# Optimization experiments

Measured on AMD Instinct MI355X. Metric: run time of the kernel, lower is better.

## Reference

```python
import jax, jax.numpy as jnp
import numpy as np

B, H, W, C = 16, 128, 128, 128
Wh = Ww = 8
SH = 4  # shift size
NH = 4  # heads
HD = C // NH
N = Wh * Ww
HID = 4 * C
EPS = 1e-3  # keras LayerNormalization default epsilon
SCALE = HD ** -0.5


def _rel_pos_index():
    coords = np.stack(np.meshgrid(np.arange(Wh), np.arange(Ww), indexing='ij'))  # (2,Wh,Ww)
    flat = coords.reshape(2, -1)
    rel = flat[:, :, None] - flat[:, None, :]  # (2,N,N)
    rel = rel.transpose(1, 2, 0) + np.array([Wh - 1, Ww - 1])
    rel = rel * np.array([2 * Ww - 1, 1])
    return rel.sum(-1).astype(np.int32)  # (N,N)


def _attn_mask():
    img = np.zeros((1, H, W, 1))
    h_sl = (slice(0, H - Wh), slice(H - Wh, H - SH), slice(H - SH, H))
    w_sl = (slice(0, W - Ww), slice(W - Ww, W - SH), slice(W - SH, W))
    cnt = 0
    for hs in h_sl:
        for ws in w_sl:
            img[:, hs, ws, :] = cnt
            cnt += 1
    mw = img.reshape(1, H // Wh, Wh, W // Ww, Ww, 1).transpose(0, 1, 3, 2, 4, 5).reshape(-1, N)
    am = mw[:, None, :] - mw[:, :, None]
    return np.where(am != 0, -100.0, 0.0).astype(np.float32)  # (nW,N,N)


def setup_inputs() -> dict:
    key = jax.random.key(0)
    ks = jax.random.split(key, 12)
    s = 0.02
    return {
        'x': jax.random.normal(ks[0], (B, H * W, C), jnp.float32),
        'w_qkv': jax.random.normal(ks[1], (C, 3 * C), jnp.float32) * s,
        'b_qkv': jnp.zeros((3 * C,), jnp.float32),
        'bias_table': jax.random.normal(ks[2], ((2 * Wh - 1) * (2 * Ww - 1), NH), jnp.float32) * s,
        'w_proj': jax.random.normal(ks[3], (C, C), jnp.float32) * s,
        'b_proj': jnp.zeros((C,), jnp.float32),
        'g1': jnp.ones((C,), jnp.float32),
        'be1': jnp.zeros((C,), jnp.float32),
        'w_fc1': jax.random.normal(ks[4], (C, HID), jnp.float32) * s,
        'b_fc1': jnp.zeros((HID,), jnp.float32),
        'w_fc2': jax.random.normal(ks[5], (HID, C), jnp.float32) * s,
        'b_fc2': jnp.zeros((C,), jnp.float32),
        'g2': jnp.ones((C,), jnp.float32),
        'be2': jnp.zeros((C,), jnp.float32),
        'rel_index': jnp.asarray(_rel_pos_index()),
        'attn_mask': jnp.asarray(_attn_mask()),
    }


def _ln(x, g, b):
    m = jnp.mean(x, -1, keepdims=True)
    v = jnp.mean(jnp.square(x - m), -1, keepdims=True)
    return (x - m) * jax.lax.rsqrt(v + EPS) * g + b


def _block(x, w_qkv, b_qkv, bias_table, w_proj, b_proj, g1, be1,
           w_fc1, b_fc1, w_fc2, b_fc2, g2, be2, rel_index, attn_mask):
    xi = x.reshape(B, H, W, C)
    xs = jnp.roll(xi, (-SH, -SH), axis=(1, 2))
    # window partition -> (B*nW, N, C)
    xw = xs.reshape(B, H // Wh, Wh, W // Ww, Ww, C).transpose(0, 1, 3, 2, 4, 5).reshape(-1, N, C)
    qkv = (xw @ w_qkv + b_qkv).reshape(-1, N, 3, NH, HD).transpose(2, 0, 3, 1, 4)
    q, k, v = qkv[0] * SCALE, qkv[1], qkv[2]
    attn = jnp.einsum('bhnd,bhmd->bhnm', q, k)  # (B*nW, NH, N, N)
    rpb = bias_table[rel_index.reshape(-1)].reshape(N, N, NH).transpose(2, 0, 1)
    attn = attn + rpb[None]
    nW = attn_mask.shape[0]
    attn = attn.reshape(-1, nW, NH, N, N) + attn_mask[None, :, None]
    attn = jax.nn.softmax(attn.reshape(-1, NH, N, N), axis=-1)
    out = jnp.einsum('bhnm,bhmd->bhnd', attn, v).transpose(0, 2, 1, 3).reshape(-1, N, C)
    out = out @ w_proj + b_proj
    # window reverse + unshift
    out = out.reshape(B, H // Wh, W // Ww, Wh, Ww, C).transpose(0, 1, 3, 2, 4, 5).reshape(B, H, W, C)
    out = jnp.roll(out, (SH, SH), axis=(1, 2)).reshape(B, H * W, C)
    # NOTE: this module applies norm AFTER the sublayers (post-norm residual)
    x = x + _ln(out, g1, be1)
    h = jax.nn.gelu(x @ w_fc1 + b_fc1, approximate=False) @ w_fc2 + b_fc2
    x = x + _ln(h, g2, be2)
    return x


def reference(x, w_qkv, b_qkv, bias_table, w_proj, b_proj, g1, be1,
              w_fc1, b_fc1, w_fc2, b_fc2, g2, be2, rel_index, attn_mask):
    return _block(x, w_qkv, b_qkv, bias_table, w_proj, b_proj, g1, be1,
                  w_fc1, b_fc1, w_fc2, b_fc2, g2, be2, rel_index, attn_mask)
```

## Files before the change

kernel.cpp:

```cpp
#include <hip/hip_runtime.h>
#include <hip/hip_bf16.h>
#include <math.h>

typedef unsigned short u16;
typedef unsigned int   u32;

typedef __bf16 bf16x8 __attribute__((ext_vector_type(8)));
typedef float  f32x4  __attribute__((ext_vector_type(4)));
#define MFMA_B16 __builtin_amdgcn_mfma_f32_16x16x32_bf16

__device__ __forceinline__ u16 f2b(float f) {
    union { float f; u32 i; } v; v.f = f;
    u32 x = v.i;
    u32 r = x + 0x7fffu + ((x >> 16) & 1u);
    return (u16)(r >> 16);
}
__device__ __forceinline__ u32 pk2(float a, float b) {
    return (u32)f2b(a) | ((u32)f2b(b) << 16);
}
__device__ __forceinline__ bf16x8 pk8(float4 f0, float4 f1) {
    union { u32 u[4]; bf16x8 v; } cv;
    cv.u[0] = pk2(f0.x, f0.y); cv.u[1] = pk2(f0.z, f0.w);
    cv.u[2] = pk2(f1.x, f1.y); cv.u[3] = pk2(f1.z, f1.w);
    return cv.v;
}

__device__ __forceinline__ float gelu_fast(float v) {
    const float z = v * (1.5957691f + 0.07135486f * v * v);
    return v * __builtin_amdgcn_rcpf(1.0f + __expf(-z));
}

#define SCALE_ 0.17677669529663687f
#define EPS_   1e-3f


__global__ __launch_bounds__(256) void swin_prep(
    const float* __restrict__ w_qkv, const float* __restrict__ w_proj,
    const float* __restrict__ w_fc1, const float* __restrict__ w_fc2,
    const float* __restrict__ bias_table, const int* __restrict__ rel_index,
    const float* __restrict__ attn_mask,
    u16* __restrict__ wqkvT, u16* __restrict__ wprojT,
    u16* __restrict__ w1T, u16* __restrict__ w2T, float* __restrict__ rpbm)
{
    const int idx = blockIdx.x * 256 + threadIdx.x;
    if (idx < 49152) {
        const int o = idx >> 7, c = idx & 127;
        wqkvT[idx] = f2b(w_qkv[c * 384 + o]);
    } else if (idx < 65536) {
        const int i2 = idx - 49152;
        const int o = i2 >> 7, c = i2 & 127;
        wprojT[i2] = f2b(w_proj[c * 128 + o]);
    } else if (idx < 131072) {
        const int i2 = idx - 65536;
        const int o = i2 >> 7, c = i2 & 127;
        w1T[i2] = f2b(w_fc1[c * 512 + o]);
    } else if (idx < 196608) {
        const int i2 = idx - 131072;
        const int o = i2 >> 9, u = i2 & 511;
        w2T[i2] = f2b(w_fc2[u * 128 + o]);
    } else if (idx < 262144) {
        const int i2 = idx - 196608;
        const int cls = i2 >> 14, rem = i2 & 16383;
        const int h = rem >> 12, ij = rem & 4095;
        const int widx = ((cls & 2) ? 240 : 0) + ((cls & 1) ? 15 : 0);
        rpbm[i2] = bias_table[rel_index[ij] * 4 + h] + attn_mask[widx * 4096 + ij];
    }
}

#define QA_OFF 0
#define KA_OFF 10240
#define VA_OFF 20480
#define PA_OFF 0
#define AO_OFF 0
#define X2F_OFF 4352

__global__ __launch_bounds__(256) void swin_attn_mfma(
    const float* __restrict__ x, const u16* __restrict__ wqkvT, const float* __restrict__ b_qkv,
    const u16* __restrict__ wprojT, const float* __restrict__ b_proj,
    const float* __restrict__ g1, const float* __restrict__ be1,
    const float* __restrict__ rpbm, float* __restrict__ x1out)
{
    __shared__ __align__(16) u16 sm[29696];
    const int tid  = threadIdx.x;
    const int w    = tid >> 6;
    const int lane = tid & 63;
    const int l15  = lane & 15;
    const int quad = lane >> 4;
    const int win  = blockIdx.x;
    const int b = win >> 8, wr = (win >> 4) & 15, wc = win & 15;

    size_t rowb[4];
    #pragma unroll
    for (int mi = 0; mi < 4; mi++) {
        const int t  = mi * 16 + l15;
        const int hh = (wr * 8 + (t >> 3) + 4) & 127;
        const int ww = (wc * 8 + (t & 7) + 4) & 127;
        rowb[mi] = ((size_t)((b * 128 + hh) * 128 + ww)) * 128;
    }

    {
        f32x4 acc[6][4];
        #pragma unroll
        for (int n = 0; n < 6; n++) {
            const float bq = b_qkv[w * 96 + n * 16 + l15];
            #pragma unroll
            for (int mi = 0; mi < 4; mi++) acc[n][mi] = (f32x4){bq, bq, bq, bq};
        }
        #pragma unroll
        for (int ks = 0; ks < 4; ks++) {
            bf16x8 a[4], bb[6];
            #pragma unroll
            for (int mi = 0; mi < 4; mi++) {
                const float4 f0 = *(const float4*)(x + rowb[mi] + ks * 32 + quad * 8);
                const float4 f1 = *(const float4*)(x + rowb[mi] + ks * 32 + quad * 8 + 4);
                a[mi] = pk8(f0, f1);
            }
            #pragma unroll
            for (int n = 0; n < 6; n++)
                bb[n] = *(const bf16x8*)(wqkvT + (size_t)(w * 96 + n * 16 + l15) * 128 + ks * 32 + quad * 8);
            #pragma unroll
            for (int n = 0; n < 6; n++)
                #pragma unroll
                for (int mi = 0; mi < 4; mi++)
                    acc[n][mi] = MFMA_B16(a[mi], bb[n], acc[n][mi], 0, 0, 0);
        }
        #pragma unroll
        for (int n = 0; n < 6; n++) {
            const int o = w * 96 + n * 16 + l15;
            const int s = o >> 7, h = (o >> 5) & 3, d = o & 31;
            #pragma unroll
            for (int mi = 0; mi < 4; mi++) {
                if (s < 2) {
                    const int base = (s ? KA_OFF : QA_OFF) + h * 2560 + d;
                    const float sc = s ? 1.0f : SCALE_;
                    #pragma unroll
                    for (int r = 0; r < 4; r++)
                        sm[base + (mi * 16 + quad * 4 + r) * 40] = f2b(acc[n][mi][r] * sc);
                } else {
                    const int t0 = mi * 16 + quad * 4;
                    const u32 w0 = pk2(acc[n][mi][0], acc[n][mi][1]);
                    const u32 w1 = pk2(acc[n][mi][2], acc[n][mi][3]);
                    *(uint2*)(sm + VA_OFF + h * 2304 + d * 72 + t0) = make_uint2(w0, w1);
                }
            }
        }
    }
    __syncthreads();

    float sinv[4][4];
    {
        const int h = w;
        const float* rb = rpbm + (size_t)((((wr == 15) ? 2 : 0) | ((wc == 15) ? 1 : 0)) * 4 + h) * 4096;
        f32x4 S[4][4];
        #pragma unroll
        for (int mi = 0; mi < 4; mi++)
            #pragma unroll
            for (int ni = 0; ni < 4; ni++)
                #pragma unroll
                for (int r = 0; r < 4; r++)
                    S[mi][ni][r] = rb[(mi * 16 + quad * 4 + r) * 64 + ni * 16 + l15];
        bf16x8 aq[4], bk[4];
        #pragma unroll
        for (int mi = 0; mi < 4; mi++)
            aq[mi] = *(const bf16x8*)(sm + QA_OFF + h * 2560 + (mi * 16 + l15) * 40 + quad * 8);
        #pragma unroll
        for (int ni = 0; ni < 4; ni++)
            bk[ni] = *(const bf16x8*)(sm + KA_OFF + h * 2560 + (ni * 16 + l15) * 40 + quad * 8);
        #pragma unroll
        for (int mi = 0; mi < 4; mi++)
            #pragma unroll
            for (int ni = 0; ni < 4; ni++)
                S[mi][ni] = MFMA_B16(aq[mi], bk[ni], S[mi][ni], 0, 0, 0);
        #pragma unroll
        for (int mi = 0; mi < 4; mi++) {
            #pragma unroll
            for (int r = 0; r < 4; r++) {
                float m0 = fmaxf(fmaxf(S[mi][0][r], S[mi][1][r]), fmaxf(S[mi][2][r], S[mi][3][r]));
                m0 = fmaxf(m0, __shfl_xor(m0, 1));
                m0 = fmaxf(m0, __shfl_xor(m0, 2));
                m0 = fmaxf(m0, __shfl_xor(m0, 4));
                m0 = fmaxf(m0, __shfl_xor(m0, 8));
                float s0 = 0.0f;
                #pragma unroll
                for (int ni = 0; ni < 4; ni++) {
                    const float e = __expf(S[mi][ni][r] - m0);
                    S[mi][ni][r] = e;
                    s0 += e;
                }
                s0 += __shfl_xor(s0, 1);
                s0 += __shfl_xor(s0, 2);
                s0 += __shfl_xor(s0, 4);
                s0 += __shfl_xor(s0, 8);
                sinv[mi][r] = __builtin_amdgcn_rcpf(s0);
            }
        }
        __syncthreads();

        #pragma unroll
        for (int mi = 0; mi < 4; mi++)
            #pragma unroll
            for (int ni = 0; ni < 4; ni++)
                #pragma unroll
                for (int r = 0; r < 4; r++)
                    sm[PA_OFF + h * 4608 + (mi * 16 + quad * 4 + r) * 72 + ni * 16 + l15] = f2b(S[mi][ni][r]);

        f32x4 O[4][2];
        #pragma unroll
        for (int mi = 0; mi < 4; mi++)
            #pragma unroll
            for (int ni = 0; ni < 2; ni++) O[mi][ni] = (f32x4){0.f, 0.f, 0.f, 0.f};
        #pragma unroll
        for (int ks = 0; ks < 2; ks++) {
            bf16x8 ap[4], bv[2];
            #pragma unroll
            for (int mi = 0; mi < 4; mi++)
                ap[mi] = *(const bf16x8*)(sm + PA_OFF + h * 4608 + (mi * 16 + l15) * 72 + ks * 32 + quad * 8);
            #pragma unroll
            for (int ni = 0; ni < 2; ni++)
                bv[ni] = *(const bf16x8*)(sm + VA_OFF + h * 2304 + (ni * 16 + l15) * 72 + ks * 32 + quad * 8);
            #pragma unroll
            for (int mi = 0; mi < 4; mi++)
                #pragma unroll
                for (int ni = 0; ni < 2; ni++)
                    O[mi][ni] = MFMA_B16(ap[mi], bv[ni], O[mi][ni], 0, 0, 0);
        }
        __syncthreads();

        #pragma unroll
        for (int mi = 0; mi < 4; mi++)
            #pragma unroll
            for (int ni = 0; ni < 2; ni++)
                #pragma unroll
                for (int r = 0; r < 4; r++)
                    sm[AO_OFF + (mi * 16 + quad * 4 + r) * 136 + h * 32 + ni * 16 + l15]
                        = f2b(O[mi][ni][r] * sinv[mi][r]);
    }
    __syncthreads();

    {
        f32x4 X2[4][2];
        #pragma unroll
        for (int ni = 0; ni < 2; ni++) {
            const float bp = b_proj[w * 32 + ni * 16 + l15];
            #pragma unroll
            for (int mi = 0; mi < 4; mi++) X2[mi][ni] = (f32x4){bp, bp, bp, bp};
        }
        #pragma unroll
        for (int ks = 0; ks < 4; ks++) {
            bf16x8 aa[4], bw[2];
            #pragma unroll
            for (int mi = 0; mi < 4; mi++)
                aa[mi] = *(const bf16x8*)(sm + AO_OFF + (mi * 16 + l15) * 136 + ks * 32 + quad * 8);
            #pragma unroll
            for (int ni = 0; ni < 2; ni++)
                bw[ni] = *(const bf16x8*)(wprojT + (size_t)(w * 32 + ni * 16 + l15) * 128 + ks * 32 + quad * 8);
            #pragma unroll
            for (int mi = 0; mi < 4; mi++)
                #pragma unroll
                for (int ni = 0; ni < 2; ni++)
                    X2[mi][ni] = MFMA_B16(aa[mi], bw[ni], X2[mi][ni], 0, 0, 0);
        }
        float* X2f = (float*)sm + X2F_OFF;
        #pragma unroll
        for (int mi = 0; mi < 4; mi++)
            #pragma unroll
            for (int ni = 0; ni < 2; ni++)
                #pragma unroll
                for (int r = 0; r < 4; r++)
                    X2f[(mi * 16 + quad * 4 + r) * 132 + w * 32 + ni * 16 + l15] = X2[mi][ni][r];
    }
    __syncthreads();

    {
        const int t = tid >> 2, part = tid & 3;
        const float* Xr = (const float*)sm + X2F_OFF + t * 132 + part * 32;
        float4 xr[8];
        float s1 = 0.f, s2 = 0.f;
        #pragma unroll
        for (int k = 0; k < 8; k++) {
            xr[k] = *(const float4*)(Xr + k * 4);
            s1 += xr[k].x + xr[k].y + xr[k].z + xr[k].w;
            s2 += xr[k].x * xr[k].x + xr[k].y * xr[k].y
                + xr[k].z * xr[k].z + xr[k].w * xr[k].w;
        }
        s1 += __shfl_xor(s1, 1); s1 += __shfl_xor(s1, 2);
        s2 += __shfl_xor(s2, 1); s2 += __shfl_xor(s2, 2);
        const float m  = s1 * 0.0078125f;
        const float vr = fmaxf(s2 * 0.0078125f - m * m, 0.f);
        const float rs = rsqrtf(vr + EPS_);
        const int hh = (wr * 8 + (t >> 3) + 4) & 127;
        const int ww = (wc * 8 + (t & 7) + 4) & 127;
        const size_t g = ((size_t)((b * 128 + hh) * 128 + ww)) * 128 + part * 32;
        #pragma unroll
        for (int k = 0; k < 8; k++) {
            const int c4 = k * 4;
            const float4 xv = *(const float4*)(x + g + c4);
            const float4 gv = *(const float4*)(g1 + part * 32 + c4);
            const float4 bv = *(const float4*)(be1 + part * 32 + c4);
            float4 o;
            o.x = xv.x + (xr[k].x - m) * rs * gv.x + bv.x;
            o.y = xv.y + (xr[k].y - m) * rs * gv.y + bv.y;
            o.z = xv.z + (xr[k].z - m) * rs * gv.z + bv.z;
            o.w = xv.w + (xr[k].w - m) * rs * gv.w + bv.w;
            *(float4*)(x1out + g + c4) = o;
        }
    }
}

#define HB_OFF 8704
#define X3F_OFF 4352

__global__ __launch_bounds__(256) void swin_mlp_mfma(
    float* __restrict__ x1io, const u16* __restrict__ w1T, const float* __restrict__ b_fc1,
    const u16* __restrict__ w2T, const float* __restrict__ b_fc2,
    const float* __restrict__ g2, const float* __restrict__ be2)
{
    __shared__ __align__(16) u16 sm[25600];
    const int tid  = threadIdx.x;
    const int w    = tid >> 6;
    const int lane = tid & 63;
    const int l15  = lane & 15;
    const int quad = lane >> 4;
    const size_t base = (size_t)blockIdx.x * 8192;

    for (int e = tid * 8; e < 8192; e += 2048) {
        const int t = e >> 7, c = e & 127;
        const float4 f0 = *(const float4*)(x1io + base + e);
        const float4 f1 = *(const float4*)(x1io + base + e + 4);
        union { bf16x8 v; uint4 u; } cv; cv.v = pk8(f0, f1);
        *(uint4*)(sm + t * 136 + c) = cv.u;
    }
    __syncthreads();

    f32x4 acc2[2][4];
    #pragma unroll
    for (int ni = 0; ni < 2; ni++) {
        const float bb = b_fc2[w * 32 + ni * 16 + l15];
        #pragma unroll
        for (int mi = 0; mi < 4; mi++) acc2[ni][mi] = (f32x4){bb, bb, bb, bb};
    }

    for (int ch = 0; ch < 2; ch++) {
        f32x4 a1[4][4];
        #pragma unroll
        for (int ni = 0; ni < 4; ni++) {
            const float bb = b_fc1[ch * 256 + (w * 4 + ni) * 16 + l15];
            #pragma unroll
            for (int mi = 0; mi < 4; mi++) a1[ni][mi] = (f32x4){bb, bb, bb, bb};
        }
        #pragma unroll
        for (int ks = 0; ks < 4; ks++) {
            bf16x8 af[4], bf[4];
            #pragma unroll
            for (int mi = 0; mi < 4; mi++)
                af[mi] = *(const bf16x8*)(sm + (mi * 16 + l15) * 136 + ks * 32 + quad * 8);
            #pragma unroll
            for (int ni = 0; ni < 4; ni++)
                bf[ni] = *(const bf16x8*)(w1T + (size_t)(ch * 256 + (w * 4 + ni) * 16 + l15) * 128 + ks * 32 + quad * 8);
            #pragma unroll
            for (int ni = 0; ni < 4; ni++)
                #pragma unroll
                for (int mi = 0; mi < 4; mi++)
                    a1[ni][mi] = MFMA_B16(af[mi], bf[ni], a1[ni][mi], 0, 0, 0);
        }
        #pragma unroll
        for (int ni = 0; ni < 4; ni++)
            #pragma unroll
            for (int mi = 0; mi < 4; mi++)
                #pragma unroll
                for (int r = 0; r < 4; r++) {
                    const float v = gelu_fast(a1[ni][mi][r]);
                    sm[HB_OFF + (mi * 16 + quad * 4 + r) * 264 + (w * 4 + ni) * 16 + l15] = f2b(v);
                }
        __syncthreads();
        #pragma unroll
        for (int ks = 0; ks < 8; ks++) {
            bf16x8 ah[4], bh[2];
            #pragma unroll
            for (int mi = 0; mi < 4; mi++)
                ah[mi] = *(const bf16x8*)(sm + HB_OFF + (mi * 16 + l15) * 264 + ks * 32 + quad * 8);
            #pragma unroll
            for (int ni = 0; ni < 2; ni++)
                bh[ni] = *(const bf16x8*)(w2T + (size_t)(w * 32 + ni * 16 + l15) * 512 + ch * 256 + ks * 32 + quad * 8);
            #pragma unroll
            for (int ni = 0; ni < 2; ni++)
                #pragma unroll
                for (int mi = 0; mi < 4; mi++)
                    acc2[ni][mi] = MFMA_B16(ah[mi], bh[ni], acc2[ni][mi], 0, 0, 0);
        }
        __syncthreads();
    }

    {
        float* X3 = (float*)sm + X3F_OFF;
        #pragma unroll
        for (int ni = 0; ni < 2; ni++)
            #pragma unroll
            for (int mi = 0; mi < 4; mi++)
                #pragma unroll
                for (int r = 0; r < 4; r++)
                    X3[(mi * 16 + quad * 4 + r) * 132 + w * 32 + ni * 16 + l15] = acc2[ni][mi][r];
    }
    __syncthreads();

    {
        const int t = tid >> 2, part = tid & 3;
        const float* Xr = (const float*)sm + X3F_OFF + t * 132 + part * 32;
        float4 xr[8];
        float s1 = 0.f, s2 = 0.f;
        #pragma unroll
        for (int k = 0; k < 8; k++) {
            xr[k] = *(const float4*)(Xr + k * 4);
            s1 += xr[k].x + xr[k].y + xr[k].z + xr[k].w;
            s2 += xr[k].x * xr[k].x + xr[k].y * xr[k].y
                + xr[k].z * xr[k].z + xr[k].w * xr[k].w;
        }
        s1 += __shfl_xor(s1, 1); s1 += __shfl_xor(s1, 2);
        s2 += __shfl_xor(s2, 1); s2 += __shfl_xor(s2, 2);
        const float m  = s1 * 0.0078125f;
        const float vr = fmaxf(s2 * 0.0078125f - m * m, 0.f);
        const float rs = rsqrtf(vr + EPS_);
        const size_t g = base + t * 128 + part * 32;
        #pragma unroll
        for (int k = 0; k < 8; k++) {
            const int c4 = k * 4;
            const float4 xv = *(const float4*)(x1io + g + c4);
            const float4 gv = *(const float4*)(g2 + part * 32 + c4);
            const float4 bv = *(const float4*)(be2 + part * 32 + c4);
            float4 o;
            o.x = xv.x + (xr[k].x - m) * rs * gv.x + bv.x;
            o.y = xv.y + (xr[k].y - m) * rs * gv.y + bv.y;
            o.z = xv.z + (xr[k].z - m) * rs * gv.z + bv.z;
            o.w = xv.w + (xr[k].w - m) * rs * gv.w + bv.w;
            *(float4*)(x1io + g + c4) = o;
        }
    }
}

extern "C" void kernel_launch(void* const* d_in, const int* in_sizes, int n_in,
                              void* d_out, int out_size, void* d_ws, size_t ws_size,
                              hipStream_t stream) {
    const float* x         = (const float*)d_in[0];
    const float* w_qkv     = (const float*)d_in[1];
    const float* b_qkv     = (const float*)d_in[2];
    const float* bias_tab  = (const float*)d_in[3];
    const float* w_proj    = (const float*)d_in[4];
    const float* b_proj    = (const float*)d_in[5];
    const float* g1        = (const float*)d_in[6];
    const float* be1       = (const float*)d_in[7];
    const float* w_fc1     = (const float*)d_in[8];
    const float* b_fc1     = (const float*)d_in[9];
    const float* w_fc2     = (const float*)d_in[10];
    const float* b_fc2     = (const float*)d_in[11];
    const float* g2        = (const float*)d_in[12];
    const float* be2       = (const float*)d_in[13];
    const int* rel_index   = (const int*)d_in[14];
    const float* attn_mask = (const float*)d_in[15];

    char* ws = (char*)d_ws;
    u16*   wqkvT  = (u16*)ws;
    u16*   wprojT = (u16*)(ws + 98304);
    u16*   w1T    = (u16*)(ws + 131072);
    u16*   w2T    = (u16*)(ws + 262144);
    float* rpbm   = (float*)(ws + 393216);

    float* x1 = (float*)d_out;

    swin_prep<<<1024, 256, 0, stream>>>(w_qkv, w_proj, w_fc1, w_fc2,
                                        bias_tab, rel_index, attn_mask,
                                        wqkvT, wprojT, w1T, w2T, rpbm);
    swin_attn_mfma<<<4096, 256, 0, stream>>>(x, wqkvT, b_qkv, wprojT, b_proj,
                                             g1, be1, rpbm, x1);
    swin_mlp_mfma<<<4096, 256, 0, stream>>>(x1, w1T, b_fc1, w2T, b_fc2, g2, be2);
}
```

Before: 740.3 us.

## Swizzle attention LDS layouts and shrink MLP hidden chunk to raise occupancy

The attention kernel drops padded Q/K/P rows in favour of XOR-swizzled layouts, which cuts its LDS footprint, and requests 3 blocks per CU through launch bounds. The MLP kernel processes the hidden dimension in four 128-wide chunks instead of two 256-wide ones. That shrinks the hidden buffer and register accumulators, so 4 blocks per CU can fit. The cost is more barriers and more chunk iterations in the MLP, and possible register spills under the tighter launch bounds. The MLP's final X3 staging now reuses LDS offset 0, which is safe only if the input tile is no longer needed by then.

Result: faster. 663.7 us (-10.3%).

```diff
diff --git a/kernel.cpp b/kernel.cpp
--- a/kernel.cpp
+++ b/kernel.cpp
@@ -28,6 +28,13 @@
 __device__ __forceinline__ float gelu_fast(float v) {
     const float z = v * (1.5957691f + 0.07135486f * v * v);
     return v * __builtin_amdgcn_rcpf(1.0f + __expf(-z));
+}
+
+__device__ __forceinline__ int qk_idx(int row, int d) {
+    return row * 32 + (d ^ (((row >> 1) & 3) << 3));
+}
+__device__ __forceinline__ int p_idx(int row, int col) {
+    return row * 64 + (col ^ ((row & 7) << 3));
 }
 
 #define SCALE_ 0.17677669529663687f
@@ -67,20 +74,20 @@
     }
 }
 
-#define QA_OFF 0
-#define KA_OFF 10240
-#define VA_OFF 20480
-#define PA_OFF 0
-#define AO_OFF 0
+#define QA_OFF  0
+#define KA_OFF  8192
+#define VA_OFF  16384
+#define PA_OFF  0
+#define AO_OFF  0
 #define X2F_OFF 4352
 
-__global__ __launch_bounds__(256) void swin_attn_mfma(
+__global__ __launch_bounds__(256, 3) void swin_attn_mfma(
     const float* __restrict__ x, const u16* __restrict__ wqkvT, const float* __restrict__ b_qkv,
     const u16* __restrict__ wprojT, const float* __restrict__ b_proj,
     const float* __restrict__ g1, const float* __restrict__ be1,
     const float* __restrict__ rpbm, float* __restrict__ x1out)
 {
-    __shared__ __align__(16) u16 sm[29696];
+    __shared__ __align__(16) u16 sm[25600];
     const int tid  = threadIdx.x;
     const int w    = tid >> 6;
     const int lane = tid & 63;
@@ -131,11 +138,13 @@
             #pragma unroll
             for (int mi = 0; mi < 4; mi++) {
                 if (s < 2) {
-                    const int base = (s ? KA_OFF : QA_OFF) + h * 2560 + d;
+                    const int base = (s ? KA_OFF : QA_OFF) + h * 2048;
                     const float sc = s ? 1.0f : SCALE_;
                     #pragma unroll
-                    for (int r = 0; r < 4; r++)
-                        sm[base + (mi * 16 + quad * 4 + r) * 40] = f2b(acc[n][mi][r] * sc);
+                    for (int r = 0; r < 4; r++) {
+                        const int row = mi * 16 + quad * 4 + r;
+                        sm[base + qk_idx(row, d)] = f2b(acc[n][mi][r] * sc);
+                    }
                 } else {
                     const int t0 = mi * 16 + quad * 4;
                     const u32 w0 = pk2(acc[n][mi][0], acc[n][mi][1]);
@@ -162,10 +171,10 @@
         bf16x8 aq[4], bk[4];
         #pragma unroll
         for (int mi = 0; mi < 4; mi++)
-            aq[mi] = *(const bf16x8*)(sm + QA_OFF + h * 2560 + (mi * 16 + l15) * 40 + quad * 8);
+            aq[mi] = *(const bf16x8*)(sm + QA_OFF + h * 2048 + qk_idx(mi * 16 + l15, quad * 8));
         #pragma unroll
         for (int ni = 0; ni < 4; ni++)
-            bk[ni] = *(const bf16x8*)(sm + KA_OFF + h * 2560 + (ni * 16 + l15) * 40 + quad * 8);
+            bk[ni] = *(const bf16x8*)(sm + KA_OFF + h * 2048 + qk_idx(ni * 16 + l15, quad * 8));
         #pragma unroll
         for (int mi = 0; mi < 4; mi++)
             #pragma unroll
@@ -202,7 +211,7 @@
             for (int ni = 0; ni < 4; ni++)
                 #pragma unroll
                 for (int r = 0; r < 4; r++)
-                    sm[PA_OFF + h * 4608 + (mi * 16 + quad * 4 + r) * 72 + ni * 16 + l15] = f2b(S[mi][ni][r]);
+                    sm[PA_OFF + h * 4096 + p_idx(mi * 16 + quad * 4 + r, ni * 16 + l15)] = f2b(S[mi][ni][r]);
 
         f32x4 O[4][2];
         #pragma unroll
@@ -214,7 +223,7 @@
             bf16x8 ap[4], bv[2];
             #pragma unroll
             for (int mi = 0; mi < 4; mi++)
-                ap[mi] = *(const bf16x8*)(sm + PA_OFF + h * 4608 + (mi * 16 + l15) * 72 + ks * 32 + quad * 8);
+                ap[mi] = *(const bf16x8*)(sm + PA_OFF + h * 4096 + p_idx(mi * 16 + l15, ks * 32 + quad * 8));
             #pragma unroll
             for (int ni = 0; ni < 2; ni++)
                 bv[ni] = *(const bf16x8*)(sm + VA_OFF + h * 2304 + (ni * 16 + l15) * 72 + ks * 32 + quad * 8);
@@ -308,14 +317,13 @@
 }
 
 #define HB_OFF 8704
-#define X3F_OFF 4352
-
-__global__ __launch_bounds__(256) void swin_mlp_mfma(
+
+__global__ __launch_bounds__(256, 4) void swin_mlp_mfma(
     float* __restrict__ x1io, const u16* __restrict__ w1T, const float* __restrict__ b_fc1,
     const u16* __restrict__ w2T, const float* __restrict__ b_fc2,
     const float* __restrict__ g2, const float* __restrict__ be2)
 {
-    __shared__ __align__(16) u16 sm[25600];
+    __shared__ __align__(16) u16 sm[17408];
     const int tid  = threadIdx.x;
     const int w    = tid >> 6;
     const int lane = tid & 63;
@@ -340,48 +348,48 @@
         for (int mi = 0; mi < 4; mi++) acc2[ni][mi] = (f32x4){bb, bb, bb, bb};
     }
 
-    for (int ch = 0; ch < 2; ch++) {
-        f32x4 a1[4][4];
-        #pragma unroll
-        for (int ni = 0; ni < 4; ni++) {
-            const float bb = b_fc1[ch * 256 + (w * 4 + ni) * 16 + l15];
+    for (int ch = 0; ch < 4; ch++) {
+        f32x4 a1[2][4];
+        #pragma unroll
+        for (int ni = 0; ni < 2; ni++) {
+            const float bb = b_fc1[ch * 128 + (w * 2 + ni) * 16 + l15];
             #pragma unroll
             for (int mi = 0; mi < 4; mi++) a1[ni][mi] = (f32x4){bb, bb, bb, bb};
         }
         #pragma unroll
         for (int ks = 0; ks < 4; ks++) {
-            bf16x8 af[4], bf[4];
+            bf16x8 af[4], bf[2];
             #pragma unroll
             for (int mi = 0; mi < 4; mi++)
                 af[mi] = *(const bf16x8*)(sm + (mi * 16 + l15) * 136 + ks * 32 + quad * 8);
             #pragma unroll
-            for (int ni = 0; ni < 4; ni++)
-                bf[ni] = *(const bf16x8*)(w1T + (size_t)(ch * 256 + (w * 4 + ni) * 16 + l15) * 128 + ks * 32 + quad * 8);
-            #pragma unroll
-            for (int ni = 0; ni < 4; ni++)
+            for (int ni = 0; ni < 2; ni++)
+                bf[ni] = *(const bf16x8*)(w1T + (size_t)(ch * 128 + (w * 2 + ni) * 16 + l15) * 128 + ks * 32 + quad * 8);
+            #pragma unroll
+            for (int ni = 0; ni < 2; ni++)
                 #pragma unroll
                 for (int mi = 0; mi < 4; mi++)
                     a1[ni][mi] = MFMA_B16(af[mi], bf[ni], a1[ni][mi], 0, 0, 0);
         }
         #pragma unroll
-        for (int ni = 0; ni < 4; ni++)
+        for (int ni = 0; ni < 2; ni++)
             #pragma unroll
             for (int mi = 0; mi < 4; mi++)
                 #pragma unroll
                 for (int r = 0; r < 4; r++) {
                     const float v = gelu_fast(a1[ni][mi][r]);
-                    sm[HB_OFF + (mi * 16 + quad * 4 + r) * 264 + (w * 4 + ni) * 16 + l15] = f2b(v);
+                    sm[HB_OFF + (mi * 16 + quad * 4 + r) * 136 + (w * 2 + ni) * 16 + l15] = f2b(v);
                 }
         __syncthreads();
         #pragma unroll
-        for (int ks = 0; ks < 8; ks++) {
+        for (int ks = 0; ks < 4; ks++) {
             bf16x8 ah[4], bh[2];
             #pragma unroll
             for (int mi = 0; mi < 4; mi++)
-                ah[mi] = *(const bf16x8*)(sm + HB_OFF + (mi * 16 + l15) * 264 + ks * 32 + quad * 8);
-            #pragma unroll
-            for (int ni = 0; ni < 2; ni++)
-                bh[ni] = *(const bf16x8*)(w2T + (size_t)(w * 32 + ni * 16 + l15) * 512 + ch * 256 + ks * 32 + quad * 8);
+                ah[mi] = *(const bf16x8*)(sm + HB_OFF + (mi * 16 + l15) * 136 + ks * 32 + quad * 8);
+            #pragma unroll
+            for (int ni = 0; ni < 2; ni++)
+                bh[ni] = *(const bf16x8*)(w2T + (size_t)(w * 32 + ni * 16 + l15) * 512 + ch * 128 + ks * 32 + quad * 8);
             #pragma unroll
             for (int ni = 0; ni < 2; ni++)
                 #pragma unroll
@@ -392,7 +400,7 @@
     }
 
     {
-        float* X3 = (float*)sm + X3F_OFF;
+        float* X3 = (float*)sm;
         #pragma unroll
         for (int ni = 0; ni < 2; ni++)
             #pragma unroll
@@ -405,7 +413,7 @@
 
     {
         const int t = tid >> 2, part = tid & 3;
-        const float* Xr = (const float*)sm + X3F_OFF + t * 132 + part * 32;
+        const float* Xr = (const float*)sm + t * 132 + part * 32;
         float4 xr[8];
         float s1 = 0.f, s2 = 0.f;
         #pragma unroll
```
